# Kernel optimization log

Hardware: AMD Instinct MI355X
Metric: run time of the kernel (lower is better)

## Reference

```python
import jax, jax.numpy as jnp
import numpy as np

B, T, D, H = 512, 256, 81, 128


def setup_inputs() -> dict:
    key = jax.random.key(0)
    ks = jax.random.split(key, 10)
    s = lambda *sh: 1.0 / np.sqrt(sh[-1])
    X_input = jax.random.normal(ks[0], (B, T, D), dtype=jnp.float32)
    # attention MLP: Linear(2H -> H), Tanh, Linear(H -> D)
    W1 = jax.random.uniform(ks[1], (H, 2 * H), jnp.float32, -s(2 * H), s(2 * H))
    b1 = jax.random.uniform(ks[2], (H,), jnp.float32, -s(2 * H), s(2 * H))
    W2 = jax.random.uniform(ks[3], (D, H), jnp.float32, -s(H), s(H))
    b2 = jax.random.uniform(ks[4], (D,), jnp.float32, -s(H), s(H))
    # single-layer LSTM, PyTorch gate order (i, f, g, o)
    W_ih = jax.random.uniform(ks[5], (4 * H, D), jnp.float32, -s(H), s(H))
    W_hh = jax.random.uniform(ks[6], (4 * H, H), jnp.float32, -s(H), s(H))
    b_ih = jax.random.uniform(ks[7], (4 * H,), jnp.float32, -s(H), s(H))
    b_hh = jax.random.uniform(ks[8], (4 * H,), jnp.float32, -s(H), s(H))
    return {"X_input": X_input, "W1": W1, "b1": b1, "W2": W2, "b2": b2,
            "W_ih": W_ih, "W_hh": W_hh, "b_ih": b_ih, "b_hh": b_hh}


def reference(X_input, W1, b1, W2, b2, W_ih, W_hh, b_ih, b_hh):
    h0 = jnp.zeros((X_input.shape[0], H), X_input.dtype)
    c0 = jnp.zeros((X_input.shape[0], H), X_input.dtype)

    def step(carry, x_t):  # x_t: [B, D]
        h, c = carry
        # input-attention MLP on cat(h_{t-1}, s_{t-1})
        hs = jnp.concatenate([h, c], axis=1)                       # [B, 2H]
        e = jnp.tanh(hs @ W1.T + b1) @ W2.T + b2                   # [B, D]
        alpha = jax.nn.softmax(e, axis=1)                          # [B, D]
        xw = alpha * x_t                                           # [B, D]
        # single LSTM cell step (PyTorch gate order i, f, g, o)
        gates = xw @ W_ih.T + b_ih + h @ W_hh.T + b_hh             # [B, 4H]
        i, f, g, o = jnp.split(gates, 4, axis=1)
        c_new = jax.nn.sigmoid(f) * c + jax.nn.sigmoid(i) * jnp.tanh(g)
        h_new = jax.nn.sigmoid(o) * jnp.tanh(c_new)
        return (h_new, c_new), (h_new, alpha)

    (_, _), (hs, alphas) = jax.lax.scan(step, (h0, c0), jnp.swapaxes(X_input, 0, 1))
    encoder_hidden_states = jnp.swapaxes(hs, 0, 1)   # [B, T, H]
    all_alpha_t = jnp.swapaxes(alphas, 0, 1)         # [B, T, D]
    return encoder_hidden_states, all_alpha_t
```

## Files before the change

### kernel.cpp

```cpp
#include <hip/hip_runtime.h>
#include <math.h>

#define BB 512
#define TT 256
#define DD 81
#define HH 128

typedef _Float16 half8 __attribute__((ext_vector_type(8)));
typedef float    f32x4 __attribute__((ext_vector_type(4)));

#define BLOB_LDS_ELEMS 5632
#define BLOB_W4_ELEMS  14336
#define BLOB_W4_OFF    BLOB_LDS_ELEMS
#define WS_ELEMS       (BLOB_LDS_ELEMS + BLOB_W4_ELEMS)

#define W1_OFF   0
#define W2_OFF   65536
#define HS_OFF   90112
#define ACT_OFF  91136
#define A1_OFF   92032
#define E_OFF    92544
#define GATE_OFF 93312
#define C_OFF    97408
#define LDS_BYTES 98432

__device__ __forceinline__ float wave_sum(float v) {
#pragma unroll
    for (int off = 32; off > 0; off >>= 1) v += __shfl_xor(v, off, 64);
    return v;
}
__device__ __forceinline__ float wave_max(float v) {
#pragma unroll
    for (int off = 32; off > 0; off >>= 1) v = fmaxf(v, __shfl_xor(v, off, 64));
    return v;
}
__device__ __forceinline__ float fast_sig(float x)  { return 1.f / (1.f + __expf(-x)); }
__device__ __forceinline__ float fast_tanh(float x) { return 1.f - 2.f / (__expf(2.f * x) + 1.f); }

__device__ __forceinline__ float4 pack8h(const float* v) {
    union { float4 f4; _Float16 h[8]; } u;
#pragma unroll
    for (int c = 0; c < 8; ++c) u.h[c] = (_Float16)v[c];
    return u.f4;
}

__global__ void repack_lds_blob(const float* __restrict__ W1, const float* __restrict__ W2,
                                float4* __restrict__ dst) {
    int tid = blockIdx.x * blockDim.x + threadIdx.x;
    if (tid >= BLOB_LDS_ELEMS) return;
    float v[8];
    if (tid < 4096) {
        int c = tid >> 6, l = tid & 63;
        int nt = c >> 3, kt = c & 7;
        int n = 16 * nt + (l & 15);
        int kb = 32 * kt + ((l >> 4) << 3);
#pragma unroll
        for (int c2 = 0; c2 < 8; ++c2) v[c2] = W1[(size_t)n * 256 + kb + c2];
    } else {
        int idx = tid - 4096;
        int c = idx >> 6, l = idx & 63;
        int nt = c >> 2, kt = c & 3;
        int n = 16 * nt + (l & 15);
        int kb = 32 * kt + ((l >> 4) << 3);
#pragma unroll
        for (int c2 = 0; c2 < 8; ++c2)
            v[c2] = (n < 81) ? W2[(size_t)n * 128 + kb + c2] : 0.f;
    }
    dst[tid] = pack8h(v);
}

__global__ void repack_w4(const float* __restrict__ Wih, const float* __restrict__ Whh,
                          const float* __restrict__ bih, const float* __restrict__ bhh,
                          float4* __restrict__ dst) {
    int tid = blockIdx.x * blockDim.x + threadIdx.x;
    if (tid >= BLOB_W4_ELEMS) return;
    int f = tid >> 9, r = tid & 511;
    int w = r >> 6, l = r & 63;
    int j = f / 7, kt = f - 7 * j;
    int n = 64 * w + 16 * j + (l & 15);
    int kb = 32 * kt + ((l >> 4) << 3);
    float v[8];
#pragma unroll
    for (int c = 0; c < 8; ++c) {
        int k = kb + c;
        float x;
        if (k < 81)        x = Wih[(size_t)n * 81 + k];
        else if (k < 209)  x = Whh[(size_t)n * 128 + (k - 81)];
        else if (k == 209) x = bih[n] + bhh[n];
        else               x = 0.f;
        v[c] = x;
    }
    dst[tid] = pack8h(v);
}

__global__ __launch_bounds__(512, 2)
void encoder_kernel(const float* __restrict__ X,
                    const float* __restrict__ b1, const float* __restrict__ b2,
                    const float4* __restrict__ wlds, const float4* __restrict__ w4q,
                    float* __restrict__ out_h, float* __restrict__ out_alpha) {
    const int tid = threadIdx.x;
    const int w   = tid >> 6;
    const int l   = tid & 63;
    const int b0  = blockIdx.x * 2;

    __shared__ __align__(16) unsigned char lds[LDS_BYTES];

#pragma unroll
    for (int i = 0; i < 11; ++i)
        ((float4*)lds)[i * 512 + tid] = wlds[i * 512 + tid];

    half8 wf[4][7];
#pragma unroll
    for (int j = 0; j < 4; ++j)
#pragma unroll
        for (int kt = 0; kt < 7; ++kt) {
            float4 t = w4q[(j * 7 + kt) * 512 + tid];
            wf[j][kt] = *(half8*)&t;
        }

    const float breg1 = b1[16 * w + (l & 15)];
    const int   n2    = 16 * w + (l & 15);
    const float breg2 = (n2 < 81) ? b2[n2] : 0.f;

    if (tid < 512) ((unsigned short*)(lds + HS_OFF))[tid] = 0;
    if (tid < 448) {
        int r = tid / 224, i = tid - r * 224;
        ((_Float16*)(lds + ACT_OFF))[r * 224 + i] = (i == 209) ? (_Float16)1.0f : (_Float16)0.0f;
    }
    if (tid < 256) ((float*)(lds + C_OFF))[tid] = 0.f;
    __syncthreads();

#pragma unroll 1
    for (int t = 0; t < TT; ++t) {
        float xv0 = 0.f, xv1 = 0.f;
        if (w < 2) {
            const float* xr = X + ((size_t)(b0 + w) * TT + t) * DD;
            xv0 = xr[l];
            if (l < DD - 64) xv1 = xr[l + 64];
        }

        {
            const unsigned offA = (l & 1) * 512 + (l >> 4) * 16;
            f32x4 ae = {0.f, 0.f, 0.f, 0.f}, ao = {0.f, 0.f, 0.f, 0.f};
#pragma unroll
            for (int kt = 0; kt < 8; ++kt) {
                half8 a = *(const half8*)(lds + HS_OFF + offA + kt * 64);
                half8 b = *(const half8*)(lds + W1_OFF + (w * 8 + kt) * 1024 + l * 16);
                if (kt & 1) ao = __builtin_amdgcn_mfma_f32_16x16x32_f16(a, b, ao, 0, 0, 0);
                else        ae = __builtin_amdgcn_mfma_f32_16x16x32_f16(a, b, ae, 0, 0, 0);
            }
            if (l < 16) {
                _Float16* a1f = (_Float16*)(lds + A1_OFF);
                float v0 = fast_tanh(ae[0] + ao[0] + breg1);
                float v1 = fast_tanh(ae[1] + ao[1] + breg1);
                a1f[16 * w + l]       = (_Float16)v0;
                a1f[128 + 16 * w + l] = (_Float16)v1;
            }
        }
        __syncthreads();

        if (w < 6) {
            const unsigned offA = (l & 1) * 256 + (l >> 4) * 16;
            f32x4 ae = {0.f, 0.f, 0.f, 0.f}, ao = {0.f, 0.f, 0.f, 0.f};
#pragma unroll
            for (int kt = 0; kt < 4; ++kt) {
                half8 a = *(const half8*)(lds + A1_OFF + offA + kt * 64);
                half8 b = *(const half8*)(lds + W2_OFF + (w * 4 + kt) * 1024 + l * 16);
                if (kt & 1) ao = __builtin_amdgcn_mfma_f32_16x16x32_f16(a, b, ao, 0, 0, 0);
                else        ae = __builtin_amdgcn_mfma_f32_16x16x32_f16(a, b, ae, 0, 0, 0);
            }
            if (l < 16) {
                float* es = (float*)(lds + E_OFF);
                es[16 * w + l]      = ae[0] + ao[0] + breg2;
                es[96 + 16 * w + l] = ae[1] + ao[1] + breg2;
            }
        }
        __syncthreads();

        if (w < 2) {
            const float* er = (const float*)(lds + E_OFF) + w * 96;
            float ev0 = er[l];
            float ev1 = (l < DD - 64) ? er[l + 64] : -INFINITY;
            float m  = wave_max(fmaxf(ev0, ev1));
            float p0 = __expf(ev0 - m);
            float p1 = (l < DD - 64) ? __expf(ev1 - m) : 0.f;
            float inv = 1.f / wave_sum(p0 + p1);
            _Float16* act = (_Float16*)(lds + ACT_OFF) + w * 224;
            float* oa = out_alpha + ((size_t)(b0 + w) * TT + t) * DD;
            float al0 = p0 * inv;
            act[l] = (_Float16)(al0 * xv0);
            oa[l] = al0;
            if (l < DD - 64) {
                float al1 = p1 * inv;
                act[l + 64] = (_Float16)(al1 * xv1);
                oa[l + 64] = al1;
            }
        }
        __syncthreads();

        {
            const unsigned offA = (l & 1) * 448 + (l >> 4) * 16;
            half8 a4[7];
#pragma unroll
            for (int kt = 0; kt < 7; ++kt)
                a4[kt] = *(const half8*)(lds + ACT_OFF + offA + kt * 64);
            f32x4 g0 = {0.f,0.f,0.f,0.f}, g1 = g0, g2 = g0, g3 = g0;
#pragma unroll
            for (int kt = 0; kt < 7; ++kt) {
                g0 = __builtin_amdgcn_mfma_f32_16x16x32_f16(a4[kt], wf[0][kt], g0, 0, 0, 0);
                g1 = __builtin_amdgcn_mfma_f32_16x16x32_f16(a4[kt], wf[1][kt], g1, 0, 0, 0);
                g2 = __builtin_amdgcn_mfma_f32_16x16x32_f16(a4[kt], wf[2][kt], g2, 0, 0, 0);
                g3 = __builtin_amdgcn_mfma_f32_16x16x32_f16(a4[kt], wf[3][kt], g3, 0, 0, 0);
            }
            if (l < 16) {
                float* gs = (float*)(lds + GATE_OFF);
                gs[       64 * w      + l] = g0[0]; gs[512 + 64 * w      + l] = g0[1];
                gs[       64 * w + 16 + l] = g1[0]; gs[512 + 64 * w + 16 + l] = g1[1];
                gs[       64 * w + 32 + l] = g2[0]; gs[512 + 64 * w + 32 + l] = g2[1];
                gs[       64 * w + 48 + l] = g3[0]; gs[512 + 64 * w + 48 + l] = g3[1];
            }
        }
        __syncthreads();

        if (tid < 256) {
            int r = tid >> 7, u = tid & 127;
            const float* gs = (const float*)(lds + GATE_OFF) + r * 512;
            float gi = gs[u], gf = gs[u + 128], gg = gs[u + 256], go = gs[u + 384];
            float* cs = (float*)(lds + C_OFF) + r * 128;
            float cn = fast_sig(gf) * cs[u] + fast_sig(gi) * fast_tanh(gg);
            float hn = fast_sig(go) * fast_tanh(cn);
            cs[u] = cn;
            _Float16 hh = (_Float16)hn, ch = (_Float16)cn;
            _Float16* hsr = (_Float16*)(lds + HS_OFF) + r * 256;
            hsr[u] = hh; hsr[128 + u] = ch;
            ((_Float16*)(lds + ACT_OFF))[r * 224 + 81 + u] = hh;
            out_h[((size_t)(b0 + r) * TT + t) * HH + u] = hn;
        }
        __syncthreads();
    }
}

extern "C" void kernel_launch(void* const* d_in, const int* in_sizes, int n_in,
                              void* d_out, int out_size, void* d_ws, size_t ws_size,
                              hipStream_t stream) {
    const float* X   = (const float*)d_in[0];
    const float* W1  = (const float*)d_in[1];
    const float* b1  = (const float*)d_in[2];
    const float* W2  = (const float*)d_in[3];
    const float* b2  = (const float*)d_in[4];
    const float* Wih = (const float*)d_in[5];
    const float* Whh = (const float*)d_in[6];
    const float* bih = (const float*)d_in[7];
    const float* bhh = (const float*)d_in[8];

    if (ws_size < (size_t)WS_ELEMS * sizeof(float4)) return;

    float4* blob = (float4*)d_ws;
    float4* wlds = blob;
    float4* w4q  = blob + BLOB_W4_OFF;

    repack_lds_blob<<<(BLOB_LDS_ELEMS + 255) / 256, 256, 0, stream>>>(W1, W2, wlds);
    repack_w4<<<(BLOB_W4_ELEMS + 255) / 256, 256, 0, stream>>>(Wih, Whh, bih, bhh, w4q);

    float* out_h     = (float*)d_out;
    float* out_alpha = (float*)d_out + (size_t)BB * TT * HH;

    encoder_kernel<<<BB / 2, 512, 0, stream>>>(X, b1, b2, wlds, w4q, out_h, out_alpha);
}
```

Before: 714.4 us.

## Restructure LSTM step to cut barriers and keep cell state in registers

Repacks W_ih/W_hh so each wave owns all four gates for the same 16 hidden units. The LSTM cell update can then run directly on MFMA accumulators with c held in registers, which removes the gate LDS round trip and one barrier. The h-part of the gate GEMM (k-tiles 3..6) is issued early alongside the W1 GEMM using a double-buffered activation row. The W2 projection and softmax are merged into two waves using 16-lane shuffles, dropping another barrier. LDS strides are padded, likely to reduce bank conflicts. The cost is more work concentrated on two waves during the attention phase and a more intricate buffer scheme.

```diff
diff --git a/kernel.cpp b/kernel.cpp
--- a/kernel.cpp
+++ b/kernel.cpp
@@ -14,26 +14,17 @@
 #define BLOB_W4_OFF    BLOB_LDS_ELEMS
 #define WS_ELEMS       (BLOB_LDS_ELEMS + BLOB_W4_ELEMS)
 
-#define W1_OFF   0
-#define W2_OFF   65536
-#define HS_OFF   90112
-#define ACT_OFF  91136
-#define A1_OFF   92032
-#define E_OFF    92544
-#define GATE_OFF 93312
-#define C_OFF    97408
-#define LDS_BYTES 98432
-
-__device__ __forceinline__ float wave_sum(float v) {
-#pragma unroll
-    for (int off = 32; off > 0; off >>= 1) v += __shfl_xor(v, off, 64);
-    return v;
-}
-__device__ __forceinline__ float wave_max(float v) {
-#pragma unroll
-    for (int off = 32; off > 0; off >>= 1) v = fmaxf(v, __shfl_xor(v, off, 64));
-    return v;
-}
+#define W1_OFF    0
+#define W2_OFF    65536
+#define HS_OFF    90112
+#define HS_STRIDE 544
+#define ACT_OFF   91200
+#define ACT_ROW   448
+#define ACT_BUF   896
+#define A1_OFF    92992
+#define A1_STRIDE 288
+#define LDS_BYTES 93568
+
 __device__ __forceinline__ float fast_sig(float x)  { return 1.f / (1.f + __expf(-x)); }
 __device__ __forceinline__ float fast_tanh(float x) { return 1.f - 2.f / (__expf(2.f * x) + 1.f); }
 
@@ -77,7 +68,7 @@
     int f = tid >> 9, r = tid & 511;
     int w = r >> 6, l = r & 63;
     int j = f / 7, kt = f - 7 * j;
-    int n = 64 * w + 16 * j + (l & 15);
+    int n = 128 * j + 16 * w + (l & 15);
     int kb = 32 * kt + ((l >> 4) << 3);
     float v[8];
 #pragma unroll
@@ -101,6 +92,7 @@
     const int tid = threadIdx.x;
     const int w   = tid >> 6;
     const int l   = tid & 63;
+    const int c16 = l & 15;
     const int b0  = blockIdx.x * 2;
 
     __shared__ __align__(16) unsigned char lds[LDS_BYTES];
@@ -118,123 +110,127 @@
             wf[j][kt] = *(half8*)&t;
         }
 
-    const float breg1 = b1[16 * w + (l & 15)];
-    const int   n2    = 16 * w + (l & 15);
-    const float breg2 = (n2 < 81) ? b2[n2] : 0.f;
-
-    if (tid < 512) ((unsigned short*)(lds + HS_OFF))[tid] = 0;
-    if (tid < 448) {
-        int r = tid / 224, i = tid - r * 224;
-        ((_Float16*)(lds + ACT_OFF))[r * 224 + i] = (i == 209) ? (_Float16)1.0f : (_Float16)0.0f;
-    }
-    if (tid < 256) ((float*)(lds + C_OFF))[tid] = 0.f;
+    const float breg1 = b1[16 * w + c16];
+    float b2q[6];
+#pragma unroll
+    for (int j = 0; j < 6; ++j) {
+        int idx = 16 * j + c16;
+        b2q[j] = (idx < DD) ? b2[idx] : 0.f;
+    }
+
+    for (int i = tid; i < (LDS_BYTES - HS_OFF) / 4; i += 512)
+        ((float*)(lds + HS_OFF))[i] = 0.f;
     __syncthreads();
+    if (tid < 4) {
+        int buf = tid >> 1, r = tid & 1;
+        ((_Float16*)(lds + ACT_OFF + buf * ACT_BUF + r * ACT_ROW))[209] = (_Float16)1.0f;
+    }
+    __syncthreads();
+
+    float c0 = 0.f, c1 = 0.f;
+    const unsigned offA_hs  = (l & 1) * HS_STRIDE + (l >> 4) * 16;
+    const unsigned offA_act = (l & 1) * ACT_ROW   + (l >> 4) * 16;
+    const unsigned offA_a1  = (l & 1) * A1_STRIDE + (l >> 4) * 16;
 
 #pragma unroll 1
     for (int t = 0; t < TT; ++t) {
-        float xv0 = 0.f, xv1 = 0.f;
+        const unsigned rbuf = (unsigned)(t & 1) * ACT_BUF;
+        const unsigned wbuf = (unsigned)((t + 1) & 1) * ACT_BUF;
+
+        float xq[6] = {0.f, 0.f, 0.f, 0.f, 0.f, 0.f};
         if (w < 2) {
             const float* xr = X + ((size_t)(b0 + w) * TT + t) * DD;
-            xv0 = xr[l];
-            if (l < DD - 64) xv1 = xr[l + 64];
-        }
-
+#pragma unroll
+            for (int j = 0; j < 5; ++j) xq[j] = xr[16 * j + c16];
+            if (c16 == 0) xq[5] = xr[80];
+        }
+
+        f32x4 g0 = {0,0,0,0}, g1 = {0,0,0,0}, g2 = {0,0,0,0}, g3 = {0,0,0,0};
         {
-            const unsigned offA = (l & 1) * 512 + (l >> 4) * 16;
-            f32x4 ae = {0.f, 0.f, 0.f, 0.f}, ao = {0.f, 0.f, 0.f, 0.f};
+            f32x4 ae = {0,0,0,0}, ao = {0,0,0,0};
 #pragma unroll
             for (int kt = 0; kt < 8; ++kt) {
-                half8 a = *(const half8*)(lds + HS_OFF + offA + kt * 64);
+                half8 a = *(const half8*)(lds + HS_OFF + offA_hs + kt * 64);
                 half8 b = *(const half8*)(lds + W1_OFF + (w * 8 + kt) * 1024 + l * 16);
                 if (kt & 1) ao = __builtin_amdgcn_mfma_f32_16x16x32_f16(a, b, ao, 0, 0, 0);
                 else        ae = __builtin_amdgcn_mfma_f32_16x16x32_f16(a, b, ae, 0, 0, 0);
             }
+#pragma unroll
+            for (int kt = 3; kt < 7; ++kt) {
+                half8 a = *(const half8*)(lds + ACT_OFF + rbuf + offA_act + kt * 64);
+                g0 = __builtin_amdgcn_mfma_f32_16x16x32_f16(a, wf[0][kt], g0, 0, 0, 0);
+                g1 = __builtin_amdgcn_mfma_f32_16x16x32_f16(a, wf[1][kt], g1, 0, 0, 0);
+                g2 = __builtin_amdgcn_mfma_f32_16x16x32_f16(a, wf[2][kt], g2, 0, 0, 0);
+                g3 = __builtin_amdgcn_mfma_f32_16x16x32_f16(a, wf[3][kt], g3, 0, 0, 0);
+            }
             if (l < 16) {
                 _Float16* a1f = (_Float16*)(lds + A1_OFF);
-                float v0 = fast_tanh(ae[0] + ao[0] + breg1);
-                float v1 = fast_tanh(ae[1] + ao[1] + breg1);
-                a1f[16 * w + l]       = (_Float16)v0;
-                a1f[128 + 16 * w + l] = (_Float16)v1;
+                a1f[16 * w + l]       = (_Float16)fast_tanh(ae[0] + ao[0] + breg1);
+                a1f[144 + 16 * w + l] = (_Float16)fast_tanh(ae[1] + ao[1] + breg1);
             }
         }
         __syncthreads();
 
-        if (w < 6) {
-            const unsigned offA = (l & 1) * 256 + (l >> 4) * 16;
-            f32x4 ae = {0.f, 0.f, 0.f, 0.f}, ao = {0.f, 0.f, 0.f, 0.f};
+        if (w < 2) {
+            f32x4 e0 = {0,0,0,0}, e1 = e0, e2v = e0, e3 = e0, e4 = e0, e5 = e0;
 #pragma unroll
             for (int kt = 0; kt < 4; ++kt) {
-                half8 a = *(const half8*)(lds + A1_OFF + offA + kt * 64);
-                half8 b = *(const half8*)(lds + W2_OFF + (w * 4 + kt) * 1024 + l * 16);
-                if (kt & 1) ao = __builtin_amdgcn_mfma_f32_16x16x32_f16(a, b, ao, 0, 0, 0);
-                else        ae = __builtin_amdgcn_mfma_f32_16x16x32_f16(a, b, ae, 0, 0, 0);
-            }
+                half8 a = *(const half8*)(lds + A1_OFF + offA_a1 + kt * 64);
+                e0  = __builtin_amdgcn_mfma_f32_16x16x32_f16(a, *(const half8*)(lds + W2_OFF + (0 * 4 + kt) * 1024 + l * 16), e0, 0, 0, 0);
+                e1  = __builtin_amdgcn_mfma_f32_16x16x32_f16(a, *(const half8*)(lds + W2_OFF + (1 * 4 + kt) * 1024 + l * 16), e1, 0, 0, 0);
+                e2v = __builtin_amdgcn_mfma_f32_16x16x32_f16(a, *(const half8*)(lds + W2_OFF + (2 * 4 + kt) * 1024 + l * 16), e2v, 0, 0, 0);
+                e3  = __builtin_amdgcn_mfma_f32_16x16x32_f16(a, *(const half8*)(lds + W2_OFF + (3 * 4 + kt) * 1024 + l * 16), e3, 0, 0, 0);
+                e4  = __builtin_amdgcn_mfma_f32_16x16x32_f16(a, *(const half8*)(lds + W2_OFF + (4 * 4 + kt) * 1024 + l * 16), e4, 0, 0, 0);
+                e5  = __builtin_amdgcn_mfma_f32_16x16x32_f16(a, *(const half8*)(lds + W2_OFF + (5 * 4 + kt) * 1024 + l * 16), e5, 0, 0, 0);
+            }
+            float ev0 = e0[w] + b2q[0], ev1 = e1[w] + b2q[1], ev2 = e2v[w] + b2q[2];
+            float ev3 = e3[w] + b2q[3], ev4 = e4[w] + b2q[4];
+            float ev5 = (c16 == 0) ? (e5[w] + b2q[5]) : -INFINITY;
+            float m = fmaxf(fmaxf(fmaxf(ev0, ev1), fmaxf(ev2, ev3)), fmaxf(ev4, ev5));
+#pragma unroll
+            for (int off = 1; off < 16; off <<= 1) m = fmaxf(m, __shfl_xor(m, off, 64));
+            float p0 = __expf(ev0 - m), p1 = __expf(ev1 - m), p2 = __expf(ev2 - m);
+            float p3 = __expf(ev3 - m), p4 = __expf(ev4 - m), p5 = __expf(ev5 - m);
+            float s = p0 + p1 + p2 + p3 + p4 + p5;
+#pragma unroll
+            for (int off = 1; off < 16; off <<= 1) s += __shfl_xor(s, off, 64);
+            float inv = 1.f / s;
             if (l < 16) {
-                float* es = (float*)(lds + E_OFF);
-                es[16 * w + l]      = ae[0] + ao[0] + breg2;
-                es[96 + 16 * w + l] = ae[1] + ao[1] + breg2;
+                float* oa = out_alpha + ((size_t)(b0 + w) * TT + t) * DD;
+                _Float16* act = (_Float16*)(lds + ACT_OFF + rbuf + w * ACT_ROW);
+                float al;
+                al = p0 * inv; oa[l]      = al; act[l]      = (_Float16)(al * xq[0]);
+                al = p1 * inv; oa[l + 16] = al; act[l + 16] = (_Float16)(al * xq[1]);
+                al = p2 * inv; oa[l + 32] = al; act[l + 32] = (_Float16)(al * xq[2]);
+                al = p3 * inv; oa[l + 48] = al; act[l + 48] = (_Float16)(al * xq[3]);
+                al = p4 * inv; oa[l + 64] = al; act[l + 64] = (_Float16)(al * xq[4]);
+                if (l == 0) { al = p5 * inv; oa[80] = al; act[80] = (_Float16)(al * xq[5]); }
             }
         }
         __syncthreads();
 
-        if (w < 2) {
-            const float* er = (const float*)(lds + E_OFF) + w * 96;
-            float ev0 = er[l];
-            float ev1 = (l < DD - 64) ? er[l + 64] : -INFINITY;
-            float m  = wave_max(fmaxf(ev0, ev1));
-            float p0 = __expf(ev0 - m);
-            float p1 = (l < DD - 64) ? __expf(ev1 - m) : 0.f;
-            float inv = 1.f / wave_sum(p0 + p1);
-            _Float16* act = (_Float16*)(lds + ACT_OFF) + w * 224;
-            float* oa = out_alpha + ((size_t)(b0 + w) * TT + t) * DD;
-            float al0 = p0 * inv;
-            act[l] = (_Float16)(al0 * xv0);
-            oa[l] = al0;
-            if (l < DD - 64) {
-                float al1 = p1 * inv;
-                act[l + 64] = (_Float16)(al1 * xv1);
-                oa[l + 64] = al1;
-            }
-        }
-        __syncthreads();
-
-        {
-            const unsigned offA = (l & 1) * 448 + (l >> 4) * 16;
-            half8 a4[7];
-#pragma unroll
-            for (int kt = 0; kt < 7; ++kt)
-                a4[kt] = *(const half8*)(lds + ACT_OFF + offA + kt * 64);
-            f32x4 g0 = {0.f,0.f,0.f,0.f}, g1 = g0, g2 = g0, g3 = g0;
-#pragma unroll
-            for (int kt = 0; kt < 7; ++kt) {
-                g0 = __builtin_amdgcn_mfma_f32_16x16x32_f16(a4[kt], wf[0][kt], g0, 0, 0, 0);
-                g1 = __builtin_amdgcn_mfma_f32_16x16x32_f16(a4[kt], wf[1][kt], g1, 0, 0, 0);
-                g2 = __builtin_amdgcn_mfma_f32_16x16x32_f16(a4[kt], wf[2][kt], g2, 0, 0, 0);
-                g3 = __builtin_amdgcn_mfma_f32_16x16x32_f16(a4[kt], wf[3][kt], g3, 0, 0, 0);
-            }
-            if (l < 16) {
-                float* gs = (float*)(lds + GATE_OFF);
-                gs[       64 * w      + l] = g0[0]; gs[512 + 64 * w      + l] = g0[1];
-                gs[       64 * w + 16 + l] = g1[0]; gs[512 + 64 * w + 16 + l] = g1[1];
-                gs[       64 * w + 32 + l] = g2[0]; gs[512 + 64 * w + 32 + l] = g2[1];
-                gs[       64 * w + 48 + l] = g3[0]; gs[512 + 64 * w + 48 + l] = g3[1];
-            }
-        }
-        __syncthreads();
-
-        if (tid < 256) {
-            int r = tid >> 7, u = tid & 127;
-            const float* gs = (const float*)(lds + GATE_OFF) + r * 512;
-            float gi = gs[u], gf = gs[u + 128], gg = gs[u + 256], go = gs[u + 384];
-            float* cs = (float*)(lds + C_OFF) + r * 128;
-            float cn = fast_sig(gf) * cs[u] + fast_sig(gi) * fast_tanh(gg);
-            float hn = fast_sig(go) * fast_tanh(cn);
-            cs[u] = cn;
-            _Float16 hh = (_Float16)hn, ch = (_Float16)cn;
-            _Float16* hsr = (_Float16*)(lds + HS_OFF) + r * 256;
-            hsr[u] = hh; hsr[128 + u] = ch;
-            ((_Float16*)(lds + ACT_OFF))[r * 224 + 81 + u] = hh;
-            out_h[((size_t)(b0 + r) * TT + t) * HH + u] = hn;
+#pragma unroll
+        for (int kt = 0; kt < 3; ++kt) {
+            half8 a = *(const half8*)(lds + ACT_OFF + rbuf + offA_act + kt * 64);
+            g0 = __builtin_amdgcn_mfma_f32_16x16x32_f16(a, wf[0][kt], g0, 0, 0, 0);
+            g1 = __builtin_amdgcn_mfma_f32_16x16x32_f16(a, wf[1][kt], g1, 0, 0, 0);
+            g2 = __builtin_amdgcn_mfma_f32_16x16x32_f16(a, wf[2][kt], g2, 0, 0, 0);
+            g3 = __builtin_amdgcn_mfma_f32_16x16x32_f16(a, wf[3][kt], g3, 0, 0, 0);
+        }
+        if (l < 16) {
+            int u = 16 * w + l;
+            c0 = fast_sig(g1[0]) * c0 + fast_sig(g0[0]) * fast_tanh(g2[0]);
+            float h0v = fast_sig(g3[0]) * fast_tanh(c0);
+            c1 = fast_sig(g1[1]) * c1 + fast_sig(g0[1]) * fast_tanh(g2[1]);
+            float h1v = fast_sig(g3[1]) * fast_tanh(c1);
+            _Float16* hsb = (_Float16*)(lds + HS_OFF);
+            hsb[u]             = (_Float16)h0v;  hsb[128 + u]       = (_Float16)c0;
+            hsb[272 + u]       = (_Float16)h1v;  hsb[272 + 128 + u] = (_Float16)c1;
+            _Float16* actw = (_Float16*)(lds + ACT_OFF + wbuf);
+            actw[81 + u]       = (_Float16)h0v;
+            actw[224 + 81 + u] = (_Float16)h1v;
+            out_h[((size_t)b0 * TT + t) * HH + u]       = h0v;
+            out_h[((size_t)(b0 + 1) * TT + t) * HH + u] = h1v;
         }
         __syncthreads();
     }
```

Measured after the change: 825.5 us. +15.5%, slower.
